# Optimization experiments

Measured on AMD Instinct MI355X. Metric: run time of the kernel, lower is better.

Reference implementation:

```python
import jax, jax.numpy as jnp
import numpy as np

RADIUS = 5.0
NB = 50                      # num_basis = radius * basis_density_per_A
SN, VN = 16, 8               # node irreps: 16x0e + 8x1o
SO, VO = 8, 4                # out  irreps:  8x0e + 4x1o
H = 128                      # MLP hidden width
NUMEL1 = SN*SN + SN*VN + VN*VN + VN*SN            # 576  (uvw paths, sh muls = 1)
NUMEL2 = SN*SN*SO + SN*VN*VO + VN*SN*VO + VN*VN*SO  # 3584
N_NODES, N_EDGES = 10000, 50000
SQ3 = 3.0 ** 0.5

# normalize2mom constant for silu (e3nn normalizes act so E[act(z)^2]=1, z~N(0,1))
_z = np.linspace(-10.0, 10.0, 40001)
_dz = _z[1] - _z[0]
_phi = np.exp(-0.5 * _z**2) / np.sqrt(2.0 * np.pi)
_s = _z / (1.0 + np.exp(-_z))
ACT_C = float(1.0 / np.sqrt(np.sum(_s * _s * _phi) * _dz))


def _mlp(x, w1, w2):
    # e3nn FullyConnectedNet: variance-preserving layers, normalized act on hidden
    h = ACT_C * jax.nn.silu(x @ (w1 / np.sqrt(w1.shape[0])))
    return h @ (w2 / np.sqrt(w2.shape[0]))


def _soft_one_hot(d):
    # soft_one_hot_linspace(basis='smooth_finite', cutoff=True)
    step = RADIUS / (NB + 1)
    values = jnp.linspace(0.0, RADIUS, NB + 2)[1:-1]
    diff = (d[:, None] - values) / step
    def sus(t):
        return jnp.where(t > 0.0, jnp.exp(-1.0 / jnp.where(t > 0.0, t, 1.0)), 0.0)
    return 1.14136 * np.exp(2.0) * sus(diff + 1.0) * sus(1.0 - diff)


def setup_inputs() -> dict:
    key = jax.random.key(0)
    ks = jax.random.split(key, 7)
    return {
        "edge_index": jax.random.randint(ks[0], (2, N_EDGES), 0, N_NODES),
        "pos": 1.5 * jax.random.normal(ks[1], (N_NODES, 3), jnp.float32),
        "x": jax.random.normal(ks[2], (N_NODES, SN + 3 * VN), jnp.float32),
        "lig_w1": jax.random.normal(ks[3], (NB, H), jnp.float32),
        "lig_w2": jax.random.normal(ks[4], (H, NUMEL1), jnp.float32),
        "rec_w1": jax.random.normal(ks[5], (NB, H), jnp.float32),
        "rec_w2": jax.random.normal(ks[6], (H, NUMEL2), jnp.float32),
    }


def reference(edge_index, pos, x, lig_w1, lig_w2, rec_w1, rec_w2):
    rec, lig = edge_index[0], edge_index[1]
    vec = pos[lig] - pos[rec]                         # [E,3]
    d = jnp.sqrt(jnp.sum(vec * vec, axis=1))
    sh1 = SQ3 * vec / jnp.maximum(d, 1e-12)[:, None]  # l=1 SH, 'component' norm; sh0 == 1
    demb = _soft_one_hot(d) * np.sqrt(NB)             # [E,NB]

    # ---- TP1: node(lig) x sh -> node, per-edge uvw weights ----
    w = _mlp(demb, lig_w1, lig_w2)                    # [E,576]
    o = 0
    W000 = w[:, o:o + SN * SN].reshape(-1, SN, SN); o += SN * SN
    W011 = w[:, o:o + SN * VN].reshape(-1, SN, VN); o += SN * VN
    W101 = w[:, o:o + VN * VN].reshape(-1, VN, VN); o += VN * VN
    W110 = w[:, o:o + VN * SN].reshape(-1, VN, SN)
    xl = x[lig]
    s1 = xl[:, :SN]
    v1 = xl[:, SN:].reshape(-1, VN, 3)
    c0 = (1.0 / (SN + VN)) ** 0.5                     # path norm, out 0e
    c1 = (3.0 / (SN + VN)) ** 0.5                     # path norm, out 1o
    v1_dot_sh = jnp.einsum('euk,ek->eu', v1, sh1)
    s_a = c0 * (jnp.einsum('euw,eu->ew', W000, s1)
                + jnp.einsum('euw,eu->ew', W110, v1_dot_sh) / SQ3)
    v_a = (c1 / SQ3) * (jnp.einsum('euw,eu,ek->ewk', W011, s1, sh1)
                        + jnp.einsum('euw,euk->ewk', W101, v1))

    # ---- TP2: msg x node(rec) -> out, per-edge uvw weights ----
    w = _mlp(demb, rec_w1, rec_w2)                    # [E,3584]
    o = 0
    W000 = w[:, o:o + SN * SN * SO].reshape(-1, SN, SN, SO); o += SN * SN * SO
    W011 = w[:, o:o + SN * VN * VO].reshape(-1, SN, VN, VO); o += SN * VN * VO
    W101 = w[:, o:o + VN * SN * VO].reshape(-1, VN, SN, VO); o += VN * SN * VO
    W110 = w[:, o:o + VN * VN * SO].reshape(-1, VN, VN, SO)
    xr = x[rec]
    s_b = xr[:, :SN]
    v_b = xr[:, SN:].reshape(-1, VN, 3)
    c0 = (1.0 / (SN * SN + VN * VN)) ** 0.5
    c1 = (3.0 / (SN * VN + VN * SN)) ** 0.5
    s_out = c0 * (jnp.einsum('euvw,eu,ev->ew', W000, s_a, s_b)
                  + jnp.einsum('euvw,euk,evk->ew', W110, v_a, v_b) / SQ3)
    v_out = (c1 / SQ3) * (jnp.einsum('euvw,eu,evk->ewk', W011, s_a, v_b)
                          + jnp.einsum('euvw,euk,ev->ewk', W101, v_a, s_b))
    return jnp.concatenate([s_out, v_out.reshape(-1, VO * 3)], axis=1)  # [E, 20]
```

## Files before the change

### kernel.cpp

```cpp
#include <hip/hip_runtime.h>
#include <math.h>

#define NE     50000
#define NNODE  10000
#define HDIM   128
#define GBIN   2048
#define NLUT   2049
#define NC     4160
#define NC1    576
#define NCHMAX 3611
#define MPAD   2064

typedef _Float16 h2 __attribute__((ext_vector_type(2)));
typedef _Float16 h8 __attribute__((ext_vector_type(8)));
typedef float f32x4 __attribute__((ext_vector_type(4)));

typedef __fp16 hp2 __attribute__((ext_vector_type(2)));
typedef __fp16 hp4 __attribute__((ext_vector_type(4)));
typedef __fp16 hp8 __attribute__((ext_vector_type(8)));

static __device__ __forceinline__ float fdot2f(hp2 p, hp2 q, float acc) {
  return __builtin_amdgcn_fdot2(p, q, acc, false);
}
static __device__ __forceinline__ hp2 pk2(float a, float b) {
  hp2 r = __builtin_amdgcn_cvt_pkrtz(a, b);
  return r;
}
static __device__ __forceinline__ hp2 mkh2(__fp16 a, __fp16 b) {
  hp2 o; o[0] = a; o[1] = b;
  return o;
}

#define SQ3C        1.7320508075688772f
#define INV_SQ3     0.5773502691896258f
#define C0_1F       0.20412414523193154f
#define C1_1_OS3F   0.20412414523193154f
#define C0_2F       0.05590169943749474f
#define C1_2_OS3F   0.0625f
#define INV_SQRT_H  0.08838834764831845f
#define DELTA       (5.0f/2048.0f)
#define INV_DELTA   409.6f
#define STEP_INV    (51.0f/5.0f)

__global__ __launch_bounds__(128) void k_hprep(
    const float* __restrict__ lw1, const float* __restrict__ rw1,
    const float actc, const float K0C,
    _Float16* __restrict__ Hl, _Float16* __restrict__ Hr) {
  const int g  = blockIdx.x;
  const int which = blockIdx.y;
  const int hc = threadIdx.x;
  const float* __restrict__ w1 = which ? rw1 : lw1;
  float h = 0.f;
  if (g <= GBIN) {
    const float tt = (float)g * DELTA * STEP_INV;
    const int i0 = (int)floorf(tt);
    float z = 0.f;
#pragma unroll
    for (int k = 0; k < 2; ++k) {
      const int ii = i0 + k;
      if (ii >= 1 && ii <= 50) {
        const float diff = tt - (float)ii;
        const float a = diff + 1.f, b = 1.f - diff;
        if (a > 0.f && b > 0.f) {
          const float val = K0C * __expf(-1.f / a - 1.f / b);
          z += val * w1[(ii - 1) * HDIM + hc];
        }
      }
    }
    h = actc * z / (1.f + __expf(-z)) * INV_SQRT_H;
  }
  _Float16* __restrict__ H = which ? Hr : Hl;
  H[(size_t)g * HDIM + hc] = (_Float16)h;
}

__global__ __launch_bounds__(256) void k_w2t(
    const float* __restrict__ lw2, const float* __restrict__ rw2,
    _Float16* __restrict__ w2t) {
  const int gid = blockIdx.x * 256 + threadIdx.x;
  if (gid >= 64 * NC) return;
  const int k2 = gid / NC;
  const int n  = gid - k2 * NC;
  float a, b;
  if (n < NC1) {
    a = lw2[(size_t)(2 * k2) * NC1 + n];
    b = lw2[(size_t)(2 * k2 + 1) * NC1 + n];
  } else {
    const int m = n - NC1;
    a = rw2[(size_t)(2 * k2) * 3584 + m];
    b = rw2[(size_t)(2 * k2 + 1) * 3584 + m];
  }
  h2 p; p[0] = (_Float16)a; p[1] = (_Float16)b;
  *(h2*)(w2t + (size_t)n * HDIM + 2 * k2) = p;
}

__global__ __launch_bounds__(256) void k_lutm(
    const _Float16* __restrict__ Hl, const _Float16* __restrict__ Hr,
    const _Float16* __restrict__ w2t, _Float16* __restrict__ lut) {
  const int tid = threadIdx.x;
  const int nt = blockIdx.y * 4 + (tid >> 6);
  const int mt = blockIdx.x;
  const int l  = tid & 63;
  const int rc = l & 15;
  const int kg = (l >> 4) * 8;
  const _Float16* __restrict__ Ap =
      ((nt < 36) ? Hl : Hr) + (size_t)(mt * 16 + rc) * HDIM + kg;
  const _Float16* __restrict__ Bp = w2t + (size_t)(nt * 16 + rc) * HDIM + kg;
  f32x4 acc = {0.f, 0.f, 0.f, 0.f};
#pragma unroll
  for (int kc = 0; kc < 4; ++kc) {
    h8 a = *(const h8*)(Ap + kc * 32);
    h8 b = *(const h8*)(Bp + kc * 32);
    acc = __builtin_amdgcn_mfma_f32_16x16x32_f16(a, b, acc, 0, 0, 0);
  }
#pragma unroll
  for (int r = 0; r < 4; ++r) {
    const int g = mt * 16 + (l >> 4) * 4 + r;
    if (g <= GBIN) lut[(size_t)g * NC + nt * 16 + rc] = (_Float16)acc[r];
  }
}

__global__ void k_edge(const int* __restrict__ ei, const float* __restrict__ pos,
                       float* __restrict__ out, int* __restrict__ bin_e,
                       float* __restrict__ f_e, int* __restrict__ cnt) {
  const int e = blockIdx.x * 256 + threadIdx.x;
  if (e >= NE) return;
  const int rec = ei[e], lig = ei[NE + e];
  const float ax = pos[lig * 3 + 0] - pos[rec * 3 + 0];
  const float ay = pos[lig * 3 + 1] - pos[rec * 3 + 1];
  const float az = pos[lig * 3 + 2] - pos[rec * 3 + 2];
  const float d = sqrtf(ax * ax + ay * ay + az * az);
  if (d > 0.f && d < 5.0f) {
    const float tf = d * INV_DELTA;
    int b = (int)tf;
    if (b > GBIN - 1) b = GBIN - 1;
    bin_e[e] = b;
    f_e[e] = tf - (float)b;
    atomicAdd(&cnt[b], 1);
  } else {
    bin_e[e] = -1;
    float* o = out + (size_t)e * 20;
#pragma unroll
    for (int i2 = 0; i2 < 20; ++i2) o[i2] = 0.f;
  }
}

__global__ void k_scan(const int* __restrict__ cnt, int* __restrict__ offs,
                       int* __restrict__ woff, int* __restrict__ chunk_bin,
                       int* __restrict__ chunk_start, int* __restrict__ nch) {
  __shared__ int lds[256];
  const int t = threadIdx.x;
  int loc[8];
  int s = 0;
#pragma unroll
  for (int i = 0; i < 8; ++i) { loc[i] = cnt[t * 8 + i]; s += loc[i]; }
  lds[t] = s;
  __syncthreads();
  for (int o = 1; o < 256; o <<= 1) {
    int v = 0;
    if (t >= o) v = lds[t - o];
    __syncthreads();
    lds[t] += v;
    __syncthreads();
  }
  int run = lds[t] - s;
  int runs[8];
#pragma unroll
  for (int i = 0; i < 8; ++i) {
    runs[i] = run;
    offs[t * 8 + i] = run;
    woff[t * 8 + i] = run;
    run += loc[i];
  }
  if (t == 255) offs[GBIN] = run;

  int ccnt[8];
  int csum = 0;
#pragma unroll
  for (int i = 0; i < 8; ++i) { ccnt[i] = (loc[i] + 31) >> 5; csum += ccnt[i]; }
  __syncthreads();
  lds[t] = csum;
  __syncthreads();
  for (int o = 1; o < 256; o <<= 1) {
    int v = 0;
    if (t >= o) v = lds[t - o];
    __syncthreads();
    lds[t] += v;
    __syncthreads();
  }
  int crun = lds[t] - csum;
#pragma unroll
  for (int i = 0; i < 8; ++i) {
    for (int c = 0; c < ccnt[i]; ++c) {
      chunk_bin[crun]   = t * 8 + i;
      chunk_start[crun] = runs[i] + c * 32;
      ++crun;
    }
  }
  if (t == 255) nch[0] = lds[255];
}

__global__ void k_scatter(const int* __restrict__ bin_e, int* __restrict__ woff,
                          int* __restrict__ sorted) {
  const int e = blockIdx.x * 256 + threadIdx.x;
  if (e >= NE) return;
  const int b = bin_e[e];
  if (b >= 0) {
    const int p = atomicAdd(&woff[b], 1);
    sorted[p] = e;
  }
}

__global__ __launch_bounds__(128) void k_epi(
    const _Float16* __restrict__ lut, const int* __restrict__ chunk_bin,
    const int* __restrict__ chunk_start, const int* __restrict__ offs,
    const int* __restrict__ sorted, const float* __restrict__ f_e,
    const int* __restrict__ ei, const float* __restrict__ pos,
    const float* __restrict__ x, float* __restrict__ out,
    const int* __restrict__ nch) {
  __shared__ __fp16 WP[2 * NC];
  const int bid = blockIdx.x;
  if (bid >= nch[0]) return;
  const int b     = chunk_bin[bid];
  const int start = chunk_start[bid];
  const int end0  = offs[b + 1];
  const int end   = (start + 32 < end0) ? (start + 32) : end0;
  const int tid = threadIdx.x;
  {
    const hp8* r0 = (const hp8*)(lut + (size_t)b * NC);
    const hp8* r1 = (const hp8*)(lut + (size_t)(b + 1) * NC);
    hp8* dst = (hp8*)WP;
    for (int i = tid; i < NC / 8; i += 128) {
      hp8 a = r0[i], c = r1[i];
      dst[2 * i]     = __builtin_shufflevector(a, c, 0, 8, 1, 9, 2, 10, 3, 11);
      dst[2 * i + 1] = __builtin_shufflevector(a, c, 4, 12, 5, 13, 6, 14, 7, 15);
    }
  }
  __syncthreads();
  const int s  = tid & 3;
  const int qb = (tid & 63) & ~3;
  const int slot = start + (tid >> 2);
  if (slot >= end) return;

  const int e = sorted[slot];
  const float f = f_e[e];
  const float fm = 1.f - f;
  const int rec = ei[e], lig = ei[NE + e];
  const float ax = pos[lig * 3 + 0] - pos[rec * 3 + 0];
  const float ay = pos[lig * 3 + 1] - pos[rec * 3 + 1];
  const float az = pos[lig * 3 + 2] - pos[rec * 3 + 2];
  const float d = sqrtf(ax * ax + ay * ay + az * az);
  const float inv = SQ3C / fmaxf(d, 1e-12f);
  const float sh0 = ax * inv, sh1 = ay * inv, sh2 = az * inv;

  float s1[16], v1[24];
  {
    const float4* xl = (const float4*)(x + (size_t)lig * 40);
#pragma unroll
    for (int j = 0; j < 4; ++j) {
      float4 v = xl[j];
      s1[j * 4 + 0] = v.x; s1[j * 4 + 1] = v.y; s1[j * 4 + 2] = v.z; s1[j * 4 + 3] = v.w;
    }
#pragma unroll
    for (int j = 0; j < 6; ++j) {
      float4 v = xl[4 + j];
      v1[j * 4 + 0] = v.x; v1[j * 4 + 1] = v.y; v1[j * 4 + 2] = v.z; v1[j * 4 + 3] = v.w;
    }
  }
  float vs[8];
#pragma unroll
  for (int u = 0; u < 8; ++u)
    vs[u] = (v1[u * 3] * sh0 + v1[u * 3 + 1] * sh1 + v1[u * 3 + 2] * sh2) * INV_SQ3;

  float A[4] = {0.f, 0.f, 0.f, 0.f};
#pragma unroll
  for (int u = 0; u < 16; ++u) {
    hp8 w = *(const hp8*)(WP + 2 * (u * 16 + s * 4));
    hp2 sp = pk2(s1[u] * fm, s1[u] * f);
    A[0] = fdot2f(mkh2(w[0], w[1]), sp, A[0]);
    A[1] = fdot2f(mkh2(w[2], w[3]), sp, A[1]);
    A[2] = fdot2f(mkh2(w[4], w[5]), sp, A[2]);
    A[3] = fdot2f(mkh2(w[6], w[7]), sp, A[3]);
  }
#pragma unroll
  for (int u = 0; u < 8; ++u) {
    hp8 w = *(const hp8*)(WP + 2 * (448 + u * 16 + s * 4));
    hp2 sp = pk2(vs[u] * fm, vs[u] * f);
    A[0] = fdot2f(mkh2(w[0], w[1]), sp, A[0]);
    A[1] = fdot2f(mkh2(w[2], w[3]), sp, A[1]);
    A[2] = fdot2f(mkh2(w[4], w[5]), sp, A[2]);
    A[3] = fdot2f(mkh2(w[6], w[7]), sp, A[3]);
  }
  const float sa0 = C0_1F * A[0];
  const float sa1 = C0_1F * A[1];
  const float sa2 = C0_1F * A[2];
  const float sa3 = C0_1F * A[3];

  float vaA0, vaA1, vaA2, vaB0, vaB1, vaB2;
  {
    float cA = 0.f, cB = 0.f;
#pragma unroll
    for (int u = 0; u < 16; ++u) {
      hp4 w = *(const hp4*)(WP + 2 * (256 + u * 8 + s * 2));
      hp2 sp = pk2(s1[u] * fm, s1[u] * f);
      cA = fdot2f(mkh2(w[0], w[1]), sp, cA);
      cB = fdot2f(mkh2(w[2], w[3]), sp, cB);
    }
    float tAx = 0.f, tAy = 0.f, tAz = 0.f, tBx = 0.f, tBy = 0.f, tBz = 0.f;
#pragma unroll
    for (int u = 0; u < 8; ++u) {
      hp4 w = *(const hp4*)(WP + 2 * (384 + u * 8 + s * 2));
      hp2 px = pk2(v1[u * 3] * fm,     v1[u * 3] * f);
      hp2 py = pk2(v1[u * 3 + 1] * fm, v1[u * 3 + 1] * f);
      hp2 pz = pk2(v1[u * 3 + 2] * fm, v1[u * 3 + 2] * f);
      hp2 pa = mkh2(w[0], w[1]);
      hp2 pb = mkh2(w[2], w[3]);
      tAx = fdot2f(pa, px, tAx); tAy = fdot2f(pa, py, tAy); tAz = fdot2f(pa, pz, tAz);
      tBx = fdot2f(pb, px, tBx); tBy = fdot2f(pb, py, tBy); tBz = fdot2f(pb, pz, tBz);
    }
    vaA0 = C1_1_OS3F * (cA * sh0 + tAx);
    vaA1 = C1_1_OS3F * (cA * sh1 + tAy);
    vaA2 = C1_1_OS3F * (cA * sh2 + tAz);
    vaB0 = C1_1_OS3F * (cB * sh0 + tBx);
    vaB1 = C1_1_OS3F * (cB * sh1 + tBy);
    vaB2 = C1_1_OS3F * (cB * sh2 + tBz);
  }

  float saF[16];
#pragma unroll
  for (int k = 0; k < 16; ++k) {
    const float v = ((k & 3) == 0) ? sa0 : ((k & 3) == 1) ? sa1 : ((k & 3) == 2) ? sa2 : sa3;
    saF[k] = __shfl(v, qb + (k >> 2), 64);
  }
  float vaF[24];
#pragma unroll
  for (int w = 0; w < 8; ++w) {
    const int src = qb + (w >> 1);
    const float x0 = (w & 1) ? vaB0 : vaA0;
    const float x1 = (w & 1) ? vaB1 : vaA1;
    const float x2 = (w & 1) ? vaB2 : vaA2;
    vaF[w * 3 + 0] = __shfl(x0, src, 64);
    vaF[w * 3 + 1] = __shfl(x1, src, 64);
    vaF[w * 3 + 2] = __shfl(x2, src, 64);
  }

  const float* xr = x + (size_t)rec * 40;
  const float sbl0 = xr[s],      sbl1 = xr[4 + s];
  const float sbl2 = xr[8 + s],  sbl3 = xr[12 + s];
  const float vbA0 = xr[16 + s * 3 + 0], vbA1 = xr[16 + s * 3 + 1], vbA2 = xr[16 + s * 3 + 2];
  const float vbB0 = xr[16 + (s + 4) * 3 + 0], vbB1 = xr[16 + (s + 4) * 3 + 1], vbB2 = xr[16 + (s + 4) * 3 + 2];

  float oe[20];

  {
    float so[8];
#pragma unroll
    for (int w = 0; w < 8; ++w) so[w] = 0.f;
#pragma unroll
    for (int u = 0; u < 16; ++u) {
      const float su = saF[u];
      const __fp16* rp = WP + 2 * (576 + u * 128 + s * 8);
#pragma unroll
      for (int vv = 0; vv < 4; ++vv) {
        const float q = su * ((vv == 0) ? sbl0 : (vv == 1) ? sbl1 : (vv == 2) ? sbl2 : sbl3);
        hp2 qp = pk2(q * fm, q * f);
        hp8 wa = *(const hp8*)(rp + 2 * (vv * 32));
        hp8 wb = *(const hp8*)(rp + 2 * (vv * 32) + 8);
        so[0] = fdot2f(mkh2(wa[0], wa[1]), qp, so[0]);
        so[1] = fdot2f(mkh2(wa[2], wa[3]), qp, so[1]);
        so[2] = fdot2f(mkh2(wa[4], wa[5]), qp, so[2]);
        so[3] = fdot2f(mkh2(wa[6], wa[7]), qp, so[3]);
        so[4] = fdot2f(mkh2(wb[0], wb[1]), qp, so[4]);
        so[5] = fdot2f(mkh2(wb[2], wb[3]), qp, so[5]);
        so[6] = fdot2f(mkh2(wb[4], wb[5]), qp, so[6]);
        so[7] = fdot2f(mkh2(wb[6], wb[7]), qp, so[7]);
      }
    }
#pragma unroll
    for (int u = 0; u < 8; ++u) {
      const float a0 = vaF[u * 3], a1 = vaF[u * 3 + 1], a2 = vaF[u * 3 + 2];
      const __fp16* rp = WP + 2 * (3648 + u * 64 + s * 8);
#pragma unroll
      for (int vv = 0; vv < 2; ++vv) {
        const float b0v = vv ? vbB0 : vbA0;
        const float b1v = vv ? vbB1 : vbA1;
        const float b2v = vv ? vbB2 : vbA2;
        const float dd = (a0 * b0v + a1 * b1v + a2 * b2v) * INV_SQ3;
        hp2 qp = pk2(dd * fm, dd * f);
        hp8 wa = *(const hp8*)(rp + 2 * (vv * 32));
        hp8 wb = *(const hp8*)(rp + 2 * (vv * 32) + 8);
        so[0] = fdot2f(mkh2(wa[0], wa[1]), qp, so[0]);
        so[1] = fdot2f(mkh2(wa[2], wa[3]), qp, so[1]);
        so[2] = fdot2f(mkh2(wa[4], wa[5]), qp, so[2]);
        so[3] = fdot2f(mkh2(wa[6], wa[7]), qp, so[3]);
        so[4] = fdot2f(mkh2(wb[0], wb[1]), qp, so[4]);
        so[5] = fdot2f(mkh2(wb[2], wb[3]), qp, so[5]);
        so[6] = fdot2f(mkh2(wb[4], wb[5]), qp, so[6]);
        so[7] = fdot2f(mkh2(wb[6], wb[7]), qp, so[7]);
      }
    }
#pragma unroll
    for (int w = 0; w < 8; ++w) oe[w] = C0_2F * so[w];
  }

  {
    float uo[12];
#pragma unroll
    for (int w = 0; w < 12; ++w) uo[w] = 0.f;
#pragma unroll
    for (int u = 0; u < 16; ++u) {
      const float su = saF[u];
      const __fp16* rp = WP + 2 * (2624 + u * 32 + s * 4);
#pragma unroll
      for (int vv = 0; vv < 2; ++vv) {
        const float q0 = su * (vv ? vbB0 : vbA0);
        const float q1 = su * (vv ? vbB1 : vbA1);
        const float q2 = su * (vv ? vbB2 : vbA2);
        hp2 q0p = pk2(q0 * fm, q0 * f);
        hp2 q1p = pk2(q1 * fm, q1 * f);
        hp2 q2p = pk2(q2 * fm, q2 * f);
        hp8 w = *(const hp8*)(rp + 2 * (vv * 16));
        hp2 p0 = mkh2(w[0], w[1]);
        hp2 p1 = mkh2(w[2], w[3]);
        hp2 p2 = mkh2(w[4], w[5]);
        hp2 p3 = mkh2(w[6], w[7]);
        uo[0] = fdot2f(p0, q0p, uo[0]); uo[1]  = fdot2f(p0, q1p, uo[1]);  uo[2]  = fdot2f(p0, q2p, uo[2]);
        uo[3] = fdot2f(p1, q0p, uo[3]); uo[4]  = fdot2f(p1, q1p, uo[4]);  uo[5]  = fdot2f(p1, q2p, uo[5]);
        uo[6] = fdot2f(p2, q0p, uo[6]); uo[7]  = fdot2f(p2, q1p, uo[7]);  uo[8]  = fdot2f(p2, q2p, uo[8]);
        uo[9] = fdot2f(p3, q0p, uo[9]); uo[10] = fdot2f(p3, q1p, uo[10]); uo[11] = fdot2f(p3, q2p, uo[11]);
      }
    }
#pragma unroll
    for (int u = 0; u < 8; ++u) {
      const float a0 = vaF[u * 3], a1 = vaF[u * 3 + 1], a2 = vaF[u * 3 + 2];
      const __fp16* rp = WP + 2 * (3136 + u * 64 + s * 4);
#pragma unroll
      for (int vv = 0; vv < 4; ++vv) {
        const float sbv = (vv == 0) ? sbl0 : (vv == 1) ? sbl1 : (vv == 2) ? sbl2 : sbl3;
        const float q0 = a0 * sbv, q1 = a1 * sbv, q2 = a2 * sbv;
        hp2 q0p = pk2(q0 * fm, q0 * f);
        hp2 q1p = pk2(q1 * fm, q1 * f);
        hp2 q2p = pk2(q2 * fm, q2 * f);
        hp8 w = *(const hp8*)(rp + 2 * (vv * 16));
        hp2 p0 = mkh2(w[0], w[1]);
        hp2 p1 = mkh2(w[2], w[3]);
        hp2 p2 = mkh2(w[4], w[5]);
        hp2 p3 = mkh2(w[6], w[7]);
        uo[0] = fdot2f(p0, q0p, uo[0]); uo[1]  = fdot2f(p0, q1p, uo[1]);  uo[2]  = fdot2f(p0, q2p, uo[2]);
        uo[3] = fdot2f(p1, q0p, uo[3]); uo[4]  = fdot2f(p1, q1p, uo[4]);  uo[5]  = fdot2f(p1, q2p, uo[5]);
        uo[6] = fdot2f(p2, q0p, uo[6]); uo[7]  = fdot2f(p2, q1p, uo[7]);  uo[8]  = fdot2f(p2, q2p, uo[8]);
        uo[9] = fdot2f(p3, q0p, uo[9]); uo[10] = fdot2f(p3, q1p, uo[10]); uo[11] = fdot2f(p3, q2p, uo[11]);
      }
    }
#pragma unroll
    for (int w = 0; w < 12; ++w) oe[8 + w] = C1_2_OS3F * uo[w];
  }

#pragma unroll
  for (int w = 0; w < 20; ++w) {
    oe[w] += __shfl_xor(oe[w], 1, 64);
    oe[w] += __shfl_xor(oe[w], 2, 64);
  }
  if (s == 0) {
    float4* op = (float4*)(out + (size_t)e * 20);
#pragma unroll
    for (int j = 0; j < 5; ++j) {
      float4 o4;
      o4.x = oe[j * 4 + 0]; o4.y = oe[j * 4 + 1];
      o4.z = oe[j * 4 + 2]; o4.w = oe[j * 4 + 3];
      op[j] = o4;
    }
  }
}

extern "C" void kernel_launch(void* const* d_in, const int* in_sizes, int n_in,
                              void* d_out, int out_size, void* d_ws, size_t ws_size,
                              hipStream_t stream) {
  const int*   ei  = (const int*)d_in[0];
  const float* pos = (const float*)d_in[1];
  const float* x   = (const float*)d_in[2];
  const float* lw1 = (const float*)d_in[3];
  const float* lw2 = (const float*)d_in[4];
  const float* rw1 = (const float*)d_in[5];
  const float* rw2 = (const float*)d_in[6];
  float* out = (float*)d_out;
  char*  ws  = (char*)d_ws;

  size_t o = 0;
  _Float16* lut = (_Float16*)(ws + o); o += (size_t)NLUT * NC * 2;
  o = (o + 15) & ~(size_t)15;
  _Float16* Hl  = (_Float16*)(ws + o); o += (size_t)MPAD * HDIM * 2;
  _Float16* Hr  = (_Float16*)(ws + o); o += (size_t)MPAD * HDIM * 2;
  _Float16* w2t = (_Float16*)(ws + o); o += (size_t)NC * HDIM * 2;
  o = (o + 15) & ~(size_t)15;
  int*   bin_e = (int*)(ws + o);  o += (size_t)NE * 4;
  float* f_e   = (float*)(ws + o); o += (size_t)NE * 4;
  int*   cnt   = (int*)(ws + o);  o += (size_t)GBIN * 4;
  int*   offs  = (int*)(ws + o);  o += (size_t)(GBIN + 1) * 4 + 12;
  int*   woff  = (int*)(ws + o);  o += (size_t)GBIN * 4;
  int*   sorted = (int*)(ws + o); o += (size_t)NE * 4;
  int*   chunk_bin   = (int*)(ws + o); o += (size_t)NCHMAX * 4;
  int*   chunk_start = (int*)(ws + o); o += (size_t)NCHMAX * 4;
  int*   nch = (int*)(ws + o); o += 16;

  double ssum = 0.0;
  const double dz = 20.0 / 40000.0;
  for (int i = 0; i <= 40000; ++i) {
    const double z = -10.0 + dz * (double)i;
    const double sil = z / (1.0 + exp(-z));
    const double phi = exp(-0.5 * z * z) / sqrt(2.0 * M_PI);
    ssum += sil * sil * phi;
  }
  const float actc = (float)(1.0 / sqrt(ssum * dz));
  const float k0c  = (float)(1.14136 * exp(2.0));

  hipMemsetAsync(cnt, 0, GBIN * 4, stream);
  k_hprep<<<dim3(MPAD, 2), 128, 0, stream>>>(lw1, rw1, actc, k0c, Hl, Hr);
  k_w2t<<<(64 * NC + 255) / 256, 256, 0, stream>>>(lw2, rw2, w2t);
  k_lutm<<<dim3(129, 65), 256, 0, stream>>>(Hl, Hr, w2t, lut);
  k_edge<<<(NE + 255) / 256, 256, 0, stream>>>(ei, pos, out, bin_e, f_e, cnt);
  k_scan<<<1, 256, 0, stream>>>(cnt, offs, woff, chunk_bin, chunk_start, nch);
  k_scatter<<<(NE + 255) / 256, 256, 0, stream>>>(bin_e, woff, sorted);
  k_epi<<<NCHMAX, 128, 0, stream>>>(lut, chunk_bin, chunk_start, offs, sorted, f_e,
                                    ei, pos, x, out, nch);
}
```

Measured before the change: 111.5 us.

## Process two edges per thread group to reuse LDS weight loads in epilogue

The epilogue kernel now uses 64-thread blocks in which each 4-lane group handles two edges (A and B) from the same 32-edge chunk. Each LDS weight fragment is loaded once and applied to both edges, halving LDS read traffic per edge. The cost is roughly double the register footprint, which may lower occupancy or cause spills. The LUT staging into shared memory is now done by half as many threads per block.

New measurement: 119.4 us. +7.1%, slower.

```diff
diff --git a/kernel.cpp b/kernel.cpp
--- a/kernel.cpp
+++ b/kernel.cpp
@@ -210,7 +210,105 @@
   }
 }
 
-__global__ __launch_bounds__(128) void k_epi(
+
+#define DO_L1(E, F, FM, SAF, VAF)                                              \
+  {                                                                            \
+    const int lig_ = ei[NE + (E)];                                             \
+    const int rec_ = ei[(E)];                                                  \
+    const float ax_ = pos[lig_ * 3 + 0] - pos[rec_ * 3 + 0];                   \
+    const float ay_ = pos[lig_ * 3 + 1] - pos[rec_ * 3 + 1];                   \
+    const float az_ = pos[lig_ * 3 + 2] - pos[rec_ * 3 + 2];                   \
+    const float d_ = sqrtf(ax_ * ax_ + ay_ * ay_ + az_ * az_);                 \
+    const float in_ = SQ3C / fmaxf(d_, 1e-12f);                                \
+    const float sh0_ = ax_ * in_, sh1_ = ay_ * in_, sh2_ = az_ * in_;          \
+    float s1_[16], v1_[24];                                                    \
+    {                                                                          \
+      const float4* xl_ = (const float4*)(x + (size_t)lig_ * 40);              \
+      _Pragma("unroll")                                                        \
+      for (int j = 0; j < 4; ++j) {                                            \
+        float4 v = xl_[j];                                                     \
+        s1_[j*4+0] = v.x; s1_[j*4+1] = v.y; s1_[j*4+2] = v.z; s1_[j*4+3] = v.w;\
+      }                                                                        \
+      _Pragma("unroll")                                                        \
+      for (int j = 0; j < 6; ++j) {                                            \
+        float4 v = xl_[4 + j];                                                 \
+        v1_[j*4+0] = v.x; v1_[j*4+1] = v.y; v1_[j*4+2] = v.z; v1_[j*4+3] = v.w;\
+      }                                                                        \
+    }                                                                          \
+    float vs_[8];                                                              \
+    _Pragma("unroll")                                                          \
+    for (int u = 0; u < 8; ++u)                                                \
+      vs_[u] = (v1_[u*3]*sh0_ + v1_[u*3+1]*sh1_ + v1_[u*3+2]*sh2_) * INV_SQ3;  \
+    float A_[4] = {0.f, 0.f, 0.f, 0.f};                                        \
+    _Pragma("unroll")                                                          \
+    for (int u = 0; u < 16; ++u) {                                             \
+      hp8 w = *(const hp8*)(WP + 2 * (u * 16 + s * 4));                        \
+      hp2 sp = pk2(s1_[u] * (FM), s1_[u] * (F));                               \
+      A_[0] = fdot2f(mkh2(w[0], w[1]), sp, A_[0]);                             \
+      A_[1] = fdot2f(mkh2(w[2], w[3]), sp, A_[1]);                             \
+      A_[2] = fdot2f(mkh2(w[4], w[5]), sp, A_[2]);                             \
+      A_[3] = fdot2f(mkh2(w[6], w[7]), sp, A_[3]);                             \
+    }                                                                          \
+    _Pragma("unroll")                                                          \
+    for (int u = 0; u < 8; ++u) {                                              \
+      hp8 w = *(const hp8*)(WP + 2 * (448 + u * 16 + s * 4));                  \
+      hp2 sp = pk2(vs_[u] * (FM), vs_[u] * (F));                               \
+      A_[0] = fdot2f(mkh2(w[0], w[1]), sp, A_[0]);                             \
+      A_[1] = fdot2f(mkh2(w[2], w[3]), sp, A_[1]);                             \
+      A_[2] = fdot2f(mkh2(w[4], w[5]), sp, A_[2]);                             \
+      A_[3] = fdot2f(mkh2(w[6], w[7]), sp, A_[3]);                             \
+    }                                                                          \
+    const float sa0_ = C0_1F * A_[0];                                          \
+    const float sa1_ = C0_1F * A_[1];                                          \
+    const float sa2_ = C0_1F * A_[2];                                          \
+    const float sa3_ = C0_1F * A_[3];                                          \
+    float cA_ = 0.f, cB_ = 0.f;                                                \
+    _Pragma("unroll")                                                          \
+    for (int u = 0; u < 16; ++u) {                                             \
+      hp4 w = *(const hp4*)(WP + 2 * (256 + u * 8 + s * 2));                   \
+      hp2 sp = pk2(s1_[u] * (FM), s1_[u] * (F));                               \
+      cA_ = fdot2f(mkh2(w[0], w[1]), sp, cA_);                                 \
+      cB_ = fdot2f(mkh2(w[2], w[3]), sp, cB_);                                 \
+    }                                                                          \
+    float tAx_=0.f, tAy_=0.f, tAz_=0.f, tBx_=0.f, tBy_=0.f, tBz_=0.f;          \
+    _Pragma("unroll")                                                          \
+    for (int u = 0; u < 8; ++u) {                                              \
+      hp4 w = *(const hp4*)(WP + 2 * (384 + u * 8 + s * 2));                   \
+      hp2 px = pk2(v1_[u*3] * (FM),     v1_[u*3] * (F));                       \
+      hp2 py = pk2(v1_[u*3+1] * (FM),   v1_[u*3+1] * (F));                     \
+      hp2 pz = pk2(v1_[u*3+2] * (FM),   v1_[u*3+2] * (F));                     \
+      hp2 pa = mkh2(w[0], w[1]);                                               \
+      hp2 pb = mkh2(w[2], w[3]);                                               \
+      tAx_ = fdot2f(pa, px, tAx_); tAy_ = fdot2f(pa, py, tAy_);                \
+      tAz_ = fdot2f(pa, pz, tAz_);                                             \
+      tBx_ = fdot2f(pb, px, tBx_); tBy_ = fdot2f(pb, py, tBy_);                \
+      tBz_ = fdot2f(pb, pz, tBz_);                                             \
+    }                                                                          \
+    const float vaA0_ = C1_1_OS3F * (cA_ * sh0_ + tAx_);                       \
+    const float vaA1_ = C1_1_OS3F * (cA_ * sh1_ + tAy_);                       \
+    const float vaA2_ = C1_1_OS3F * (cA_ * sh2_ + tAz_);                       \
+    const float vaB0_ = C1_1_OS3F * (cB_ * sh0_ + tBx_);                       \
+    const float vaB1_ = C1_1_OS3F * (cB_ * sh1_ + tBy_);                       \
+    const float vaB2_ = C1_1_OS3F * (cB_ * sh2_ + tBz_);                       \
+    _Pragma("unroll")                                                          \
+    for (int k = 0; k < 16; ++k) {                                             \
+      const float v = ((k&3)==0) ? sa0_ : ((k&3)==1) ? sa1_ :                  \
+                      ((k&3)==2) ? sa2_ : sa3_;                                \
+      SAF[k] = __shfl(v, qb + (k >> 2), 64);                                   \
+    }                                                                          \
+    _Pragma("unroll")                                                          \
+    for (int w = 0; w < 8; ++w) {                                              \
+      const int src = qb + (w >> 1);                                           \
+      const float x0 = (w & 1) ? vaB0_ : vaA0_;                                \
+      const float x1 = (w & 1) ? vaB1_ : vaA1_;                                \
+      const float x2 = (w & 1) ? vaB2_ : vaA2_;                                \
+      VAF[w*3+0] = __shfl(x0, src, 64);                                        \
+      VAF[w*3+1] = __shfl(x1, src, 64);                                        \
+      VAF[w*3+2] = __shfl(x2, src, 64);                                        \
+    }                                                                          \
+  }
+
+__global__ __launch_bounds__(64) void k_epi(
     const _Float16* __restrict__ lut, const int* __restrict__ chunk_bin,
     const int* __restrict__ chunk_start, const int* __restrict__ offs,
     const int* __restrict__ sorted, const float* __restrict__ f_e,
@@ -229,7 +327,7 @@
     const hp8* r0 = (const hp8*)(lut + (size_t)b * NC);
     const hp8* r1 = (const hp8*)(lut + (size_t)(b + 1) * NC);
     hp8* dst = (hp8*)WP;
-    for (int i = tid; i < NC / 8; i += 128) {
+    for (int i = tid; i < NC / 8; i += 64) {
       hp8 a = r0[i], c = r1[i];
       dst[2 * i]     = __builtin_shufflevector(a, c, 0, 8, 1, 9, 2, 10, 3, 11);
       dst[2 * i + 1] = __builtin_shufflevector(a, c, 4, 12, 5, 13, 6, 14, 7, 15);
@@ -237,237 +335,201 @@
   }
   __syncthreads();
   const int s  = tid & 3;
-  const int qb = (tid & 63) & ~3;
-  const int slot = start + (tid >> 2);
-  if (slot >= end) return;
-
-  const int e = sorted[slot];
-  const float f = f_e[e];
-  const float fm = 1.f - f;
-  const int rec = ei[e], lig = ei[NE + e];
-  const float ax = pos[lig * 3 + 0] - pos[rec * 3 + 0];
-  const float ay = pos[lig * 3 + 1] - pos[rec * 3 + 1];
-  const float az = pos[lig * 3 + 2] - pos[rec * 3 + 2];
-  const float d = sqrtf(ax * ax + ay * ay + az * az);
-  const float inv = SQ3C / fmaxf(d, 1e-12f);
-  const float sh0 = ax * inv, sh1 = ay * inv, sh2 = az * inv;
-
-  float s1[16], v1[24];
+  const int qb = tid & ~3;
+  const int slotA = start + 2 * (tid >> 2);
+  if (slotA >= end) return;
+  const int slotB = slotA + 1;
+  const int validB = (slotB < end);
+
+  const int eA = sorted[slotA];
+  const int eB = sorted[validB ? slotB : slotA];
+  const float fA = f_e[eA], fmA = 1.f - fA;
+  const float fB = f_e[eB], fmB = 1.f - fB;
+
+  float saFA[16], vaFA[24], saFB[16], vaFB[24];
+  DO_L1(eA, fA, fmA, saFA, vaFA);
+  DO_L1(eB, fB, fmB, saFB, vaFB);
+
+  float sblA[4], vbA[6], sblB[4], vbB[6];
   {
-    const float4* xl = (const float4*)(x + (size_t)lig * 40);
-#pragma unroll
-    for (int j = 0; j < 4; ++j) {
-      float4 v = xl[j];
-      s1[j * 4 + 0] = v.x; s1[j * 4 + 1] = v.y; s1[j * 4 + 2] = v.z; s1[j * 4 + 3] = v.w;
-    }
-#pragma unroll
-    for (int j = 0; j < 6; ++j) {
-      float4 v = xl[4 + j];
-      v1[j * 4 + 0] = v.x; v1[j * 4 + 1] = v.y; v1[j * 4 + 2] = v.z; v1[j * 4 + 3] = v.w;
-    }
-  }
-  float vs[8];
-#pragma unroll
-  for (int u = 0; u < 8; ++u)
-    vs[u] = (v1[u * 3] * sh0 + v1[u * 3 + 1] * sh1 + v1[u * 3 + 2] * sh2) * INV_SQ3;
-
-  float A[4] = {0.f, 0.f, 0.f, 0.f};
-#pragma unroll
-  for (int u = 0; u < 16; ++u) {
-    hp8 w = *(const hp8*)(WP + 2 * (u * 16 + s * 4));
-    hp2 sp = pk2(s1[u] * fm, s1[u] * f);
-    A[0] = fdot2f(mkh2(w[0], w[1]), sp, A[0]);
-    A[1] = fdot2f(mkh2(w[2], w[3]), sp, A[1]);
-    A[2] = fdot2f(mkh2(w[4], w[5]), sp, A[2]);
-    A[3] = fdot2f(mkh2(w[6], w[7]), sp, A[3]);
-  }
-#pragma unroll
-  for (int u = 0; u < 8; ++u) {
-    hp8 w = *(const hp8*)(WP + 2 * (448 + u * 16 + s * 4));
-    hp2 sp = pk2(vs[u] * fm, vs[u] * f);
-    A[0] = fdot2f(mkh2(w[0], w[1]), sp, A[0]);
-    A[1] = fdot2f(mkh2(w[2], w[3]), sp, A[1]);
-    A[2] = fdot2f(mkh2(w[4], w[5]), sp, A[2]);
-    A[3] = fdot2f(mkh2(w[6], w[7]), sp, A[3]);
-  }
-  const float sa0 = C0_1F * A[0];
-  const float sa1 = C0_1F * A[1];
-  const float sa2 = C0_1F * A[2];
-  const float sa3 = C0_1F * A[3];
-
-  float vaA0, vaA1, vaA2, vaB0, vaB1, vaB2;
+    const float* xr = x + (size_t)ei[eA] * 40;
+#pragma unroll
+    for (int j = 0; j < 4; ++j) sblA[j] = xr[j * 4 + s];
+#pragma unroll
+    for (int k = 0; k < 3; ++k) {
+      vbA[k]     = xr[16 + s * 3 + k];
+      vbA[3 + k] = xr[16 + (s + 4) * 3 + k];
+    }
+    const float* xr2 = x + (size_t)ei[eB] * 40;
+#pragma unroll
+    for (int j = 0; j < 4; ++j) sblB[j] = xr2[j * 4 + s];
+#pragma unroll
+    for (int k = 0; k < 3; ++k) {
+      vbB[k]     = xr2[16 + s * 3 + k];
+      vbB[3 + k] = xr2[16 + (s + 4) * 3 + k];
+    }
+  }
+
+  float oeA[20], oeB[20];
+
   {
-    float cA = 0.f, cB = 0.f;
+    float soA[8], soB[8];
+#pragma unroll
+    for (int w = 0; w < 8; ++w) { soA[w] = 0.f; soB[w] = 0.f; }
 #pragma unroll
     for (int u = 0; u < 16; ++u) {
-      hp4 w = *(const hp4*)(WP + 2 * (256 + u * 8 + s * 2));
-      hp2 sp = pk2(s1[u] * fm, s1[u] * f);
-      cA = fdot2f(mkh2(w[0], w[1]), sp, cA);
-      cB = fdot2f(mkh2(w[2], w[3]), sp, cB);
-    }
-    float tAx = 0.f, tAy = 0.f, tAz = 0.f, tBx = 0.f, tBy = 0.f, tBz = 0.f;
-#pragma unroll
-    for (int u = 0; u < 8; ++u) {
-      hp4 w = *(const hp4*)(WP + 2 * (384 + u * 8 + s * 2));
-      hp2 px = pk2(v1[u * 3] * fm,     v1[u * 3] * f);
-      hp2 py = pk2(v1[u * 3 + 1] * fm, v1[u * 3 + 1] * f);
-      hp2 pz = pk2(v1[u * 3 + 2] * fm, v1[u * 3 + 2] * f);
-      hp2 pa = mkh2(w[0], w[1]);
-      hp2 pb = mkh2(w[2], w[3]);
-      tAx = fdot2f(pa, px, tAx); tAy = fdot2f(pa, py, tAy); tAz = fdot2f(pa, pz, tAz);
-      tBx = fdot2f(pb, px, tBx); tBy = fdot2f(pb, py, tBy); tBz = fdot2f(pb, pz, tBz);
-    }
-    vaA0 = C1_1_OS3F * (cA * sh0 + tAx);
-    vaA1 = C1_1_OS3F * (cA * sh1 + tAy);
-    vaA2 = C1_1_OS3F * (cA * sh2 + tAz);
-    vaB0 = C1_1_OS3F * (cB * sh0 + tBx);
-    vaB1 = C1_1_OS3F * (cB * sh1 + tBy);
-    vaB2 = C1_1_OS3F * (cB * sh2 + tBz);
-  }
-
-  float saF[16];
-#pragma unroll
-  for (int k = 0; k < 16; ++k) {
-    const float v = ((k & 3) == 0) ? sa0 : ((k & 3) == 1) ? sa1 : ((k & 3) == 2) ? sa2 : sa3;
-    saF[k] = __shfl(v, qb + (k >> 2), 64);
-  }
-  float vaF[24];
-#pragma unroll
-  for (int w = 0; w < 8; ++w) {
-    const int src = qb + (w >> 1);
-    const float x0 = (w & 1) ? vaB0 : vaA0;
-    const float x1 = (w & 1) ? vaB1 : vaA1;
-    const float x2 = (w & 1) ? vaB2 : vaA2;
-    vaF[w * 3 + 0] = __shfl(x0, src, 64);
-    vaF[w * 3 + 1] = __shfl(x1, src, 64);
-    vaF[w * 3 + 2] = __shfl(x2, src, 64);
-  }
-
-  const float* xr = x + (size_t)rec * 40;
-  const float sbl0 = xr[s],      sbl1 = xr[4 + s];
-  const float sbl2 = xr[8 + s],  sbl3 = xr[12 + s];
-  const float vbA0 = xr[16 + s * 3 + 0], vbA1 = xr[16 + s * 3 + 1], vbA2 = xr[16 + s * 3 + 2];
-  const float vbB0 = xr[16 + (s + 4) * 3 + 0], vbB1 = xr[16 + (s + 4) * 3 + 1], vbB2 = xr[16 + (s + 4) * 3 + 2];
-
-  float oe[20];
-
-  {
-    float so[8];
-#pragma unroll
-    for (int w = 0; w < 8; ++w) so[w] = 0.f;
-#pragma unroll
-    for (int u = 0; u < 16; ++u) {
-      const float su = saF[u];
+      const float suA = saFA[u], suB = saFB[u];
       const __fp16* rp = WP + 2 * (576 + u * 128 + s * 8);
 #pragma unroll
       for (int vv = 0; vv < 4; ++vv) {
-        const float q = su * ((vv == 0) ? sbl0 : (vv == 1) ? sbl1 : (vv == 2) ? sbl2 : sbl3);
-        hp2 qp = pk2(q * fm, q * f);
+        const float qA = suA * sblA[vv];
+        const float qB = suB * sblB[vv];
+        hp2 qpA = pk2(qA * fmA, qA * fA);
+        hp2 qpB = pk2(qB * fmB, qB * fB);
         hp8 wa = *(const hp8*)(rp + 2 * (vv * 32));
         hp8 wb = *(const hp8*)(rp + 2 * (vv * 32) + 8);
-        so[0] = fdot2f(mkh2(wa[0], wa[1]), qp, so[0]);
-        so[1] = fdot2f(mkh2(wa[2], wa[3]), qp, so[1]);
-        so[2] = fdot2f(mkh2(wa[4], wa[5]), qp, so[2]);
-        so[3] = fdot2f(mkh2(wa[6], wa[7]), qp, so[3]);
-        so[4] = fdot2f(mkh2(wb[0], wb[1]), qp, so[4]);
-        so[5] = fdot2f(mkh2(wb[2], wb[3]), qp, so[5]);
-        so[6] = fdot2f(mkh2(wb[4], wb[5]), qp, so[6]);
-        so[7] = fdot2f(mkh2(wb[6], wb[7]), qp, so[7]);
+        hp2 p0 = mkh2(wa[0], wa[1]), p1 = mkh2(wa[2], wa[3]);
+        hp2 p2 = mkh2(wa[4], wa[5]), p3 = mkh2(wa[6], wa[7]);
+        hp2 p4 = mkh2(wb[0], wb[1]), p5 = mkh2(wb[2], wb[3]);
+        hp2 p6 = mkh2(wb[4], wb[5]), p7 = mkh2(wb[6], wb[7]);
+        soA[0] = fdot2f(p0, qpA, soA[0]); soA[1] = fdot2f(p1, qpA, soA[1]);
+        soA[2] = fdot2f(p2, qpA, soA[2]); soA[3] = fdot2f(p3, qpA, soA[3]);
+        soA[4] = fdot2f(p4, qpA, soA[4]); soA[5] = fdot2f(p5, qpA, soA[5]);
+        soA[6] = fdot2f(p6, qpA, soA[6]); soA[7] = fdot2f(p7, qpA, soA[7]);
+        soB[0] = fdot2f(p0, qpB, soB[0]); soB[1] = fdot2f(p1, qpB, soB[1]);
+        soB[2] = fdot2f(p2, qpB, soB[2]); soB[3] = fdot2f(p3, qpB, soB[3]);
+        soB[4] = fdot2f(p4, qpB, soB[4]); soB[5] = fdot2f(p5, qpB, soB[5]);
+        soB[6] = fdot2f(p6, qpB, soB[6]); soB[7] = fdot2f(p7, qpB, soB[7]);
       }
     }
 #pragma unroll
     for (int u = 0; u < 8; ++u) {
-      const float a0 = vaF[u * 3], a1 = vaF[u * 3 + 1], a2 = vaF[u * 3 + 2];
+      const float aA0 = vaFA[u*3], aA1 = vaFA[u*3+1], aA2 = vaFA[u*3+2];
+      const float aB0 = vaFB[u*3], aB1 = vaFB[u*3+1], aB2 = vaFB[u*3+2];
       const __fp16* rp = WP + 2 * (3648 + u * 64 + s * 8);
 #pragma unroll
       for (int vv = 0; vv < 2; ++vv) {
-        const float b0v = vv ? vbB0 : vbA0;
-        const float b1v = vv ? vbB1 : vbA1;
-        const float b2v = vv ? vbB2 : vbA2;
-        const float dd = (a0 * b0v + a1 * b1v + a2 * b2v) * INV_SQ3;
-        hp2 qp = pk2(dd * fm, dd * f);
+        const float dA = (aA0*vbA[vv*3] + aA1*vbA[vv*3+1] + aA2*vbA[vv*3+2]) * INV_SQ3;
+        const float dB = (aB0*vbB[vv*3] + aB1*vbB[vv*3+1] + aB2*vbB[vv*3+2]) * INV_SQ3;
+        hp2 qpA = pk2(dA * fmA, dA * fA);
+        hp2 qpB = pk2(dB * fmB, dB * fB);
         hp8 wa = *(const hp8*)(rp + 2 * (vv * 32));
         hp8 wb = *(const hp8*)(rp + 2 * (vv * 32) + 8);
-        so[0] = fdot2f(mkh2(wa[0], wa[1]), qp, so[0]);
-        so[1] = fdot2f(mkh2(wa[2], wa[3]), qp, so[1]);
-        so[2] = fdot2f(mkh2(wa[4], wa[5]), qp, so[2]);
-        so[3] = fdot2f(mkh2(wa[6], wa[7]), qp, so[3]);
-        so[4] = fdot2f(mkh2(wb[0], wb[1]), qp, so[4]);
-        so[5] = fdot2f(mkh2(wb[2], wb[3]), qp, so[5]);
-        so[6] = fdot2f(mkh2(wb[4], wb[5]), qp, so[6]);
-        so[7] = fdot2f(mkh2(wb[6], wb[7]), qp, so[7]);
+        hp2 p0 = mkh2(wa[0], wa[1]), p1 = mkh2(wa[2], wa[3]);
+        hp2 p2 = mkh2(wa[4], wa[5]), p3 = mkh2(wa[6], wa[7]);
+        hp2 p4 = mkh2(wb[0], wb[1]), p5 = mkh2(wb[2], wb[3]);
+        hp2 p6 = mkh2(wb[4], wb[5]), p7 = mkh2(wb[6], wb[7]);
+        soA[0] = fdot2f(p0, qpA, soA[0]); soA[1] = fdot2f(p1, qpA, soA[1]);
+        soA[2] = fdot2f(p2, qpA, soA[2]); soA[3] = fdot2f(p3, qpA, soA[3]);
+        soA[4] = fdot2f(p4, qpA, soA[4]); soA[5] = fdot2f(p5, qpA, soA[5]);
+        soA[6] = fdot2f(p6, qpA, soA[6]); soA[7] = fdot2f(p7, qpA, soA[7]);
+        soB[0] = fdot2f(p0, qpB, soB[0]); soB[1] = fdot2f(p1, qpB, soB[1]);
+        soB[2] = fdot2f(p2, qpB, soB[2]); soB[3] = fdot2f(p3, qpB, soB[3]);
+        soB[4] = fdot2f(p4, qpB, soB[4]); soB[5] = fdot2f(p5, qpB, soB[5]);
+        soB[6] = fdot2f(p6, qpB, soB[6]); soB[7] = fdot2f(p7, qpB, soB[7]);
       }
     }
 #pragma unroll
-    for (int w = 0; w < 8; ++w) oe[w] = C0_2F * so[w];
+    for (int w = 0; w < 8; ++w) {
+      oeA[w] = C0_2F * soA[w];
+      oeB[w] = C0_2F * soB[w];
+    }
   }
 
   {
-    float uo[12];
-#pragma unroll
-    for (int w = 0; w < 12; ++w) uo[w] = 0.f;
+    float uoA[12], uoB[12];
+#pragma unroll
+    for (int w = 0; w < 12; ++w) { uoA[w] = 0.f; uoB[w] = 0.f; }
 #pragma unroll
     for (int u = 0; u < 16; ++u) {
-      const float su = saF[u];
+      const float suA = saFA[u], suB = saFB[u];
       const __fp16* rp = WP + 2 * (2624 + u * 32 + s * 4);
 #pragma unroll
       for (int vv = 0; vv < 2; ++vv) {
-        const float q0 = su * (vv ? vbB0 : vbA0);
-        const float q1 = su * (vv ? vbB1 : vbA1);
-        const float q2 = su * (vv ? vbB2 : vbA2);
-        hp2 q0p = pk2(q0 * fm, q0 * f);
-        hp2 q1p = pk2(q1 * fm, q1 * f);
-        hp2 q2p = pk2(q2 * fm, q2 * f);
+        const float qA0 = suA * vbA[vv*3], qA1 = suA * vbA[vv*3+1], qA2 = suA * vbA[vv*3+2];
+        const float qB0 = suB * vbB[vv*3], qB1 = suB * vbB[vv*3+1], qB2 = suB * vbB[vv*3+2];
+        hp2 qA0p = pk2(qA0 * fmA, qA0 * fA);
+        hp2 qA1p = pk2(qA1 * fmA, qA1 * fA);
+        hp2 qA2p = pk2(qA2 * fmA, qA2 * fA);
+        hp2 qB0p = pk2(qB0 * fmB, qB0 * fB);
+        hp2 qB1p = pk2(qB1 * fmB, qB1 * fB);
+        hp2 qB2p = pk2(qB2 * fmB, qB2 * fB);
         hp8 w = *(const hp8*)(rp + 2 * (vv * 16));
         hp2 p0 = mkh2(w[0], w[1]);
         hp2 p1 = mkh2(w[2], w[3]);
         hp2 p2 = mkh2(w[4], w[5]);
         hp2 p3 = mkh2(w[6], w[7]);
-        uo[0] = fdot2f(p0, q0p, uo[0]); uo[1]  = fdot2f(p0, q1p, uo[1]);  uo[2]  = fdot2f(p0, q2p, uo[2]);
-        uo[3] = fdot2f(p1, q0p, uo[3]); uo[4]  = fdot2f(p1, q1p, uo[4]);  uo[5]  = fdot2f(p1, q2p, uo[5]);
-        uo[6] = fdot2f(p2, q0p, uo[6]); uo[7]  = fdot2f(p2, q1p, uo[7]);  uo[8]  = fdot2f(p2, q2p, uo[8]);
-        uo[9] = fdot2f(p3, q0p, uo[9]); uo[10] = fdot2f(p3, q1p, uo[10]); uo[11] = fdot2f(p3, q2p, uo[11]);
+        uoA[0] = fdot2f(p0, qA0p, uoA[0]); uoA[1]  = fdot2f(p0, qA1p, uoA[1]);  uoA[2]  = fdot2f(p0, qA2p, uoA[2]);
+        uoA[3] = fdot2f(p1, qA0p, uoA[3]); uoA[4]  = fdot2f(p1, qA1p, uoA[4]);  uoA[5]  = fdot2f(p1, qA2p, uoA[5]);
+        uoA[6] = fdot2f(p2, qA0p, uoA[6]); uoA[7]  = fdot2f(p2, qA1p, uoA[7]);  uoA[8]  = fdot2f(p2, qA2p, uoA[8]);
+        uoA[9] = fdot2f(p3, qA0p, uoA[9]); uoA[10] = fdot2f(p3, qA1p, uoA[10]); uoA[11] = fdot2f(p3, qA2p, uoA[11]);
+        uoB[0] = fdot2f(p0, qB0p, uoB[0]); uoB[1]  = fdot2f(p0, qB1p, uoB[1]);  uoB[2]  = fdot2f(p0, qB2p, uoB[2]);
+        uoB[3] = fdot2f(p1, qB0p, uoB[3]); uoB[4]  = fdot2f(p1, qB1p, uoB[4]);  uoB[5]  = fdot2f(p1, qB2p, uoB[5]);
+        uoB[6] = fdot2f(p2, qB0p, uoB[6]); uoB[7]  = fdot2f(p2, qB1p, uoB[7]);  uoB[8]  = fdot2f(p2, qB2p, uoB[8]);
+        uoB[9] = fdot2f(p3, qB0p, uoB[9]); uoB[10] = fdot2f(p3, qB1p, uoB[10]); uoB[11] = fdot2f(p3, qB2p, uoB[11]);
       }
     }
 #pragma unroll
     for (int u = 0; u < 8; ++u) {
-      const float a0 = vaF[u * 3], a1 = vaF[u * 3 + 1], a2 = vaF[u * 3 + 2];
+      const float aA0 = vaFA[u*3], aA1 = vaFA[u*3+1], aA2 = vaFA[u*3+2];
+      const float aB0 = vaFB[u*3], aB1 = vaFB[u*3+1], aB2 = vaFB[u*3+2];
       const __fp16* rp = WP + 2 * (3136 + u * 64 + s * 4);
 #pragma unroll
       for (int vv = 0; vv < 4; ++vv) {
-        const float sbv = (vv == 0) ? sbl0 : (vv == 1) ? sbl1 : (vv == 2) ? sbl2 : sbl3;
-        const float q0 = a0 * sbv, q1 = a1 * sbv, q2 = a2 * sbv;
-        hp2 q0p = pk2(q0 * fm, q0 * f);
-        hp2 q1p = pk2(q1 * fm, q1 * f);
-        hp2 q2p = pk2(q2 * fm, q2 * f);
+        const float sA = sblA[vv], sB = sblB[vv];
+        const float qA0 = aA0 * sA, qA1 = aA1 * sA, qA2 = aA2 * sA;
+        const float qB0 = aB0 * sB, qB1 = aB1 * sB, qB2 = aB2 * sB;
+        hp2 qA0p = pk2(qA0 * fmA, qA0 * fA);
+        hp2 qA1p = pk2(qA1 * fmA, qA1 * fA);
+        hp2 qA2p = pk2(qA2 * fmA, qA2 * fA);
+        hp2 qB0p = pk2(qB0 * fmB, qB0 * fB);
+        hp2 qB1p = pk2(qB1 * fmB, qB1 * fB);
+        hp2 qB2p = pk2(qB2 * fmB, qB2 * fB);
         hp8 w = *(const hp8*)(rp + 2 * (vv * 16));
         hp2 p0 = mkh2(w[0], w[1]);
         hp2 p1 = mkh2(w[2], w[3]);
         hp2 p2 = mkh2(w[4], w[5]);
         hp2 p3 = mkh2(w[6], w[7]);
-        uo[0] = fdot2f(p0, q0p, uo[0]); uo[1]  = fdot2f(p0, q1p, uo[1]);  uo[2]  = fdot2f(p0, q2p, uo[2]);
-        uo[3] = fdot2f(p1, q0p, uo[3]); uo[4]  = fdot2f(p1, q1p, uo[4]);  uo[5]  = fdot2f(p1, q2p, uo[5]);
-        uo[6] = fdot2f(p2, q0p, uo[6]); uo[7]  = fdot2f(p2, q1p, uo[7]);  uo[8]  = fdot2f(p2, q2p, uo[8]);
-        uo[9] = fdot2f(p3, q0p, uo[9]); uo[10] = fdot2f(p3, q1p, uo[10]); uo[11] = fdot2f(p3, q2p, uo[11]);
+        uoA[0] = fdot2f(p0, qA0p, uoA[0]); uoA[1]  = fdot2f(p0, qA1p, uoA[1]);  uoA[2]  = fdot2f(p0, qA2p, uoA[2]);
+        uoA[3] = fdot2f(p1, qA0p, uoA[3]); uoA[4]  = fdot2f(p1, qA1p, uoA[4]);  uoA[5]  = fdot2f(p1, qA2p, uoA[5]);
+        uoA[6] = fdot2f(p2, qA0p, uoA[6]); uoA[7]  = fdot2f(p2, qA1p, uoA[7]);  uoA[8]  = fdot2f(p2, qA2p, uoA[8]);
+        uoA[9] = fdot2f(p3, qA0p, uoA[9]); uoA[10] = fdot2f(p3, qA1p, uoA[10]); uoA[11] = fdot2f(p3, qA2p, uoA[11]);
+        uoB[0] = fdot2f(p0, qB0p, uoB[0]); uoB[1]  = fdot2f(p0, qB1p, uoB[1]);  uoB[2]  = fdot2f(p0, qB2p, uoB[2]);
+        uoB[3] = fdot2f(p1, qB0p, uoB[3]); uoB[4]  = fdot2f(p1, qB1p, uoB[4]);  uoB[5]  = fdot2f(p1, qB2p, uoB[5]);
+        uoB[6] = fdot2f(p2, qB0p, uoB[6]); uoB[7]  = fdot2f(p2, qB1p, uoB[7]);  uoB[8]  = fdot2f(p2, qB2p, uoB[8]);
+        uoB[9] = fdot2f(p3, qB0p, uoB[9]); uoB[10] = fdot2f(p3, qB1p, uoB[10]); uoB[11] = fdot2f(p3, qB2p, uoB[11]);
       }
     }
 #pragma unroll
-    for (int w = 0; w < 12; ++w) oe[8 + w] = C1_2_OS3F * uo[w];
+    for (int w = 0; w < 12; ++w) {
+      oeA[8 + w] = C1_2_OS3F * uoA[w];
+      oeB[8 + w] = C1_2_OS3F * uoB[w];
+    }
   }
 
 #pragma unroll
   for (int w = 0; w < 20; ++w) {
-    oe[w] += __shfl_xor(oe[w], 1, 64);
-    oe[w] += __shfl_xor(oe[w], 2, 64);
+    oeA[w] += __shfl_xor(oeA[w], 1, 64);
+    oeA[w] += __shfl_xor(oeA[w], 2, 64);
+    oeB[w] += __shfl_xor(oeB[w], 1, 64);
+    oeB[w] += __shfl_xor(oeB[w], 2, 64);
   }
   if (s == 0) {
-    float4* op = (float4*)(out + (size_t)e * 20);
+    float4* opA = (float4*)(out + (size_t)eA * 20);
 #pragma unroll
     for (int j = 0; j < 5; ++j) {
       float4 o4;
-      o4.x = oe[j * 4 + 0]; o4.y = oe[j * 4 + 1];
-      o4.z = oe[j * 4 + 2]; o4.w = oe[j * 4 + 3];
-      op[j] = o4;
+      o4.x = oeA[j*4+0]; o4.y = oeA[j*4+1]; o4.z = oeA[j*4+2]; o4.w = oeA[j*4+3];
+      opA[j] = o4;
+    }
+    if (validB) {
+      float4* opB = (float4*)(out + (size_t)eB * 20);
+#pragma unroll
+      for (int j = 0; j < 5; ++j) {
+        float4 o4;
+        o4.x = oeB[j*4+0]; o4.y = oeB[j*4+1]; o4.z = oeB[j*4+2]; o4.w = oeB[j*4+3];
+        opB[j] = o4;
+      }
     }
   }
 }
@@ -520,6 +582,6 @@
   k_edge<<<(NE + 255) / 256, 256, 0, stream>>>(ei, pos, out, bin_e, f_e, cnt);
   k_scan<<<1, 256, 0, stream>>>(cnt, offs, woff, chunk_bin, chunk_start, nch);
   k_scatter<<<(NE + 255) / 256, 256, 0, stream>>>(bin_e, woff, sorted);
-  k_epi<<<NCHMAX, 128, 0, stream>>>(lut, chunk_bin, chunk_start, offs, sorted, f_e,
-                                    ei, pos, x, out, nch);
-}
+  k_epi<<<NCHMAX, 64, 0, stream>>>(lut, chunk_bin, chunk_start, offs, sorted, f_e,
+                                   ei, pos, x, out, nch);
+}
```
